# Performance work log

Measured on AMD Instinct MI355X. Metric: run time of the kernel, lower is better.

## Reference

```python
import jax, jax.numpy as jnp
import numpy as np
from jax import lax

KS = 11          # kernel_size
SIGMA = 1.5
MAX_VAL = 1.0
K1, K2 = 0.01, 0.03


def _gauss2d(ks=KS, sigma=SIGMA):
    x = np.arange(ks, dtype=np.float64) - ks // 2
    g = np.exp(-(x ** 2) / (2.0 * sigma ** 2))
    g = g / g.sum()
    return np.outer(g, g).astype(np.float32)  # [ks, ks]


def _bilinear_matrix(n_in, n_out):
    # align_corners=True bilinear resize as a linear map [n_out, n_in]
    pos = np.arange(n_out, dtype=np.float64) * (n_in - 1) / (n_out - 1)
    i0 = np.floor(pos).astype(np.int64)
    i1 = np.minimum(i0 + 1, n_in - 1)
    w = (pos - i0).astype(np.float32)
    M = np.zeros((n_out, n_in), dtype=np.float32)
    M[np.arange(n_out), i0] += 1.0 - w
    M[np.arange(n_out), i1] += w
    return jnp.asarray(M)


def setup_inputs() -> dict:
    key = jax.random.key(0)
    k1, k2 = jax.random.split(key)
    inp = jax.random.uniform(k1, (32, 3, 384, 384), dtype=jnp.float32)
    tgt = jax.random.uniform(k2, (32, 3, 512, 512), dtype=jnp.float32)
    return {"input": inp, "target": tgt}


def _ssim_loss(input, target):
    B, C, Hi, Wi = input.shape
    Ho, Wo = target.shape[-2], target.shape[-1]
    # bilinear align_corners interpolation of input to target spatial size
    A = _bilinear_matrix(Hi, Ho)  # [Ho, Hi]
    Bm = _bilinear_matrix(Wi, Wo)  # [Wo, Wi]
    img1 = jnp.einsum('oh,bchw,pw->bcop', A, input, Bm)
    img2 = target

    w2d = jnp.asarray(_gauss2d())
    window = jnp.broadcast_to(w2d, (C, 1, KS, KS))  # depthwise kernel [C,1,k,k]

    def dwconv(x):
        return lax.conv_general_dilated(
            x, window, window_strides=(1, 1), padding='VALID',
            feature_group_count=C,
            dimension_numbers=('NCHW', 'OIHW', 'NCHW'))

    mu1 = dwconv(img1)
    mu2 = dwconv(img2)
    mu1_sq = mu1 * mu1
    mu2_sq = mu2 * mu2
    mu1_mu2 = mu1 * mu2
    sigma1_sq = dwconv(img1 * img1) - mu1_sq
    sigma2_sq = dwconv(img2 * img2) - mu2_sq
    sigma12 = dwconv(img1 * img2) - mu1_mu2

    C1 = (K1 * MAX_VAL) ** 2
    C2 = (K2 * MAX_VAL) ** 2
    v1 = 2.0 * sigma12 + C2
    v2 = sigma1_sq + sigma2_sq + C2
    ssim_map = (2.0 * mu1_mu2 + C1) * v1 / ((mu1_sq + mu2_sq + C1) * v2)
    ret = jnp.mean(ssim_map)
    return jnp.clip(1.0 - ret, 0.0, 1.0)


def reference(input, target):
    return _ssim_loss(input, target)
```

## Files before the change

### kernel.cpp

```cpp
#include <hip/hip_runtime.h>


constexpr int KS = 11;
constexpr int HI = 384, WI = 384, HO = 512, WO = 512;
constexpr int OUTD = 502;
constexpr int NPLANE = 96;
constexpr int CH_OUT = 32;
constexpr int NCHUNK = 16;
constexpr float C1 = 1.0e-4f;
constexpr float C2 = 9.0e-4f;

__device__ __constant__ float GW[KS] = {
    0.00102838f, 0.00759876f, 0.03600076f, 0.10936070f, 0.21300554f,
    0.26601172f, 0.21300554f, 0.10936070f, 0.03600076f, 0.00759876f, 0.00102838f};

__device__ __forceinline__ float4 f4fma(float w, float4 x, float4 a)
{
    a.x = fmaf(w, x.x, a.x); a.y = fmaf(w, x.y, a.y);
    a.z = fmaf(w, x.z, a.z); a.w = fmaf(w, x.w, a.w);
    return a;
}

__device__ __forceinline__ float ssim_term(float4 f)
{
    float S = f.x, D = f.y, P = f.z, M = f.w;
    float SS = S * S, DD = D * D;
    float mu12 = 0.25f * (SS - DD);
    float musq = 0.5f  * (SS + DD);
    float s12  = 0.25f * (P - M) - mu12;
    float ssum = 0.5f  * (P + M) - musq;
    float num = fmaf(2.f, mu12, C1) * fmaf(2.f, s12, C2);
    float den = (musq + C1) * (ssum + C2);
    return __fdividef(num, den);
}

__global__ __launch_bounds__(256, 2)
void ssim_stream(const float* __restrict__ input, const float* __restrict__ target,
                 double* __restrict__ accum)
{
    __shared__ __align__(16) float4 chE[2][262];
    __shared__ __align__(16) float4 chO[2][262];
    __shared__ float wave_sums[4];

    const int tid   = threadIdx.x;
    const int chunk = blockIdx.x;
    const int plane = blockIdx.y;
    const int oyb   = chunk * CH_OUT;
    const int nout  = min(CH_OUT, OUTD - oyb);
    const int rows  = nout + KS - 1;

    const int c0 = 2 * tid;

    float pA = (float)(c0 * (WI - 1)) / (float)(WO - 1);
    int   xA0 = (int)pA; float wxA = pA - (float)xA0;
    float pB = (float)((c0 + 1) * (WI - 1)) / (float)(WO - 1);
    int   xB0 = (int)pB; float wxB = pB - (float)xB0;
    const bool shift = (xB0 != xA0);
    const int xs0 = xA0, xs1 = xA0 + 1, xs2 = min(xA0 + 2, WI - 1);

    const float* __restrict__ ip = input  + (size_t)plane * HI * WI;
    const float* __restrict__ tp = target + (size_t)plane * HO * WO;

    float4 rA[11], rB[11];
    #pragma unroll
    for (int s = 0; s < 11; ++s) {
        rA[s] = make_float4(0.f, 0.f, 0.f, 0.f);
        rB[s] = make_float4(0.f, 0.f, 0.f, 0.f);
    }

    float u0[2], u1[2], u2[2], v0[2], v1[2], v2[2], wyp[2];
    float2 tg[2];
    auto PRELOAD = [&](int r, int sl) {
        int y = oyb + r;
        float py = (float)(y * (HI - 1)) / (float)(HO - 1);
        int y0 = (int)py; wyp[sl] = py - (float)y0;
        int y1 = min(y0 + 1, HI - 1);
        const float* r0 = ip + y0 * WI;
        const float* r1 = ip + y1 * WI;
        u0[sl] = r0[xs0]; u1[sl] = r0[xs1]; u2[sl] = r0[xs2];
        v0[sl] = r1[xs0]; v1[sl] = r1[xs1]; v2[sl] = r1[xs2];
        tg[sl] = *(const float2*)&tp[y * WO + c0];
    };

    float lsum = 0.f;
    PRELOAD(0, 0);
    PRELOAD(1, 1);

    for (int t = 0; t < 2; ++t) {
        #pragma unroll
        for (int i = 0; i < 22; ++i) {
            const int r = t * 22 + i;
            if (r < rows) {
                const int p = i & 1;
                float wy = wyp[p];
                float V0 = fmaf(wy, v0[p] - u0[p], u0[p]);
                float V1 = fmaf(wy, v1[p] - u1[p], u1[p]);
                float V2 = fmaf(wy, v2[p] - u2[p], u2[p]);
                float a0 = fmaf(wxA, V1 - V0, V0);
                float bL = shift ? V1 : V0;
                float bR = shift ? V2 : V1;
                float a1 = fmaf(wxB, bR - bL, bL);
                float2 tv = tg[p];
                float s0 = a0 + tv.x, d0 = a0 - tv.x;
                float s1 = a1 + tv.y, d1 = a1 - tv.y;
                chE[p][tid] = make_float4(s0, d0, s0 * s0, d0 * d0);
                chO[p][tid] = make_float4(s1, d1, s1 * s1, d1 * d1);
                if (r + 2 < rows) PRELOAD(r + 2, p);
                __syncthreads();
                float4 acc0 = make_float4(0.f, 0.f, 0.f, 0.f);
                float4 acc1 = make_float4(0.f, 0.f, 0.f, 0.f);
                #pragma unroll
                for (int m = 0; m < 6; ++m) {
                    float4 E = chE[p][tid + m];
                    float4 O = chO[p][tid + m];
                    float we = GW[2 * m];
                    acc0 = f4fma(we, E, acc0);
                    acc1 = f4fma(we, O, acc1);
                    if (m < 5) acc0 = f4fma(GW[2 * m + 1], O, acc0);
                    if (m >= 1) acc1 = f4fma(GW[2 * m - 1], E, acc1);
                }
                const int im = i % 11;
                #pragma unroll
                for (int j = 0; j < 11; ++j) {
                    const int sl = (im - j + 11) % 11;
                    rA[sl] = f4fma(GW[j], acc0, rA[sl]);
                    rB[sl] = f4fma(GW[j], acc1, rB[sl]);
                }
                const int sf = (im + 1) % 11;
                if (r >= 10) {
                    if (c0 < OUTD) {
                        lsum += ssim_term(rA[sf]);
                        if (c0 + 1 < OUTD) lsum += ssim_term(rB[sf]);
                    }
                }
                rA[sf] = make_float4(0.f, 0.f, 0.f, 0.f);
                rB[sf] = make_float4(0.f, 0.f, 0.f, 0.f);
            }
        }
    }

    #pragma unroll
    for (int off = 32; off > 0; off >>= 1) lsum += __shfl_down(lsum, off);
    int wave = tid >> 6, lane = tid & 63;
    if (lane == 0) wave_sums[wave] = lsum;
    __syncthreads();
    if (tid == 0) {
        float s = wave_sums[0] + wave_sums[1] + wave_sums[2] + wave_sums[3];
        atomicAdd(accum, (double)s);
    }
}

__global__ void ssim_finalize(const double* __restrict__ accum, float* __restrict__ out)
{
    if (threadIdx.x == 0 && blockIdx.x == 0) {
        double mean = accum[0] / ((double)NPLANE * OUTD * OUTD);
        double l = 1.0 - mean;
        if (l < 0.0) l = 0.0;
        if (l > 1.0) l = 1.0;
        out[0] = (float)l;
    }
}

extern "C" void kernel_launch(void* const* d_in, const int* in_sizes, int n_in,
                              void* d_out, int out_size, void* d_ws, size_t ws_size,
                              hipStream_t stream)
{
    const float* input  = (const float*)d_in[0];
    const float* target = (const float*)d_in[1];
    float* out = (float*)d_out;
    double* accum = (double*)d_ws;

    hipMemsetAsync(accum, 0, sizeof(double), stream);

    dim3 grid(NCHUNK, NPLANE);
    ssim_stream<<<grid, dim3(256), 0, stream>>>(input, target, accum);
    ssim_finalize<<<1, 64, 0, stream>>>(accum, out);
}
```

Before: 309.1 us.

## Do vertical blur first from a register ring, horizontal via LDS

Reorders the separable Gaussian so each thread keeps a ring of 11 raw sum/difference rows in registers and applies the vertical filter first. Only the resulting vertical sums are exchanged through LDS for the horizontal pass. This replaces the 11-slot sliding accumulator arrays (two float4 arrays) with a single float4 ring, cutting register pressure so the launch bound can ask for 4 blocks per SM instead of 2. The trade-off is that each output row now recomputes an 11-tap vertical sum including squares, and the first 10 rows skip the barrier and LDS work.

```diff
diff --git a/kernel.cpp b/kernel.cpp
--- a/kernel.cpp
+++ b/kernel.cpp
@@ -34,12 +34,12 @@
     return __fdividef(num, den);
 }
 
-__global__ __launch_bounds__(256, 2)
+__global__ __launch_bounds__(256, 4)
 void ssim_stream(const float* __restrict__ input, const float* __restrict__ target,
                  double* __restrict__ accum)
 {
-    __shared__ __align__(16) float4 chE[2][262];
-    __shared__ __align__(16) float4 chO[2][262];
+    __shared__ __align__(16) float4 hE[2][262];
+    __shared__ __align__(16) float4 hO[2][262];
     __shared__ float wave_sums[4];
 
     const int tid   = threadIdx.x;
@@ -56,17 +56,12 @@
     float pB = (float)((c0 + 1) * (WI - 1)) / (float)(WO - 1);
     int   xB0 = (int)pB; float wxB = pB - (float)xB0;
     const bool shift = (xB0 != xA0);
-    const int xs0 = xA0, xs1 = xA0 + 1, xs2 = min(xA0 + 2, WI - 1);
+    const int xs0 = xA0, xs1 = min(xA0 + 1, WI - 1), xs2 = min(xA0 + 2, WI - 1);
 
     const float* __restrict__ ip = input  + (size_t)plane * HI * WI;
     const float* __restrict__ tp = target + (size_t)plane * HO * WO;
 
-    float4 rA[11], rB[11];
-    #pragma unroll
-    for (int s = 0; s < 11; ++s) {
-        rA[s] = make_float4(0.f, 0.f, 0.f, 0.f);
-        rB[s] = make_float4(0.f, 0.f, 0.f, 0.f);
-    }
+    float4 q[11];
 
     float u0[2], u1[2], u2[2], v0[2], v1[2], v2[2], wyp[2];
     float2 tg[2];
@@ -91,7 +86,8 @@
         for (int i = 0; i < 22; ++i) {
             const int r = t * 22 + i;
             if (r < rows) {
-                const int p = i & 1;
+                const int p  = i & 1;
+                const int im = i % 11;
                 float wy = wyp[p];
                 float V0 = fmaf(wy, v0[p] - u0[p], u0[p]);
                 float V1 = fmaf(wy, v1[p] - u1[p], u1[p]);
@@ -101,40 +97,41 @@
                 float bR = shift ? V2 : V1;
                 float a1 = fmaf(wxB, bR - bL, bL);
                 float2 tv = tg[p];
-                float s0 = a0 + tv.x, d0 = a0 - tv.x;
-                float s1 = a1 + tv.y, d1 = a1 - tv.y;
-                chE[p][tid] = make_float4(s0, d0, s0 * s0, d0 * d0);
-                chO[p][tid] = make_float4(s1, d1, s1 * s1, d1 * d1);
+                q[im] = make_float4(a0 + tv.x, a0 - tv.x, a1 + tv.y, a1 - tv.y);
                 if (r + 2 < rows) PRELOAD(r + 2, p);
-                __syncthreads();
-                float4 acc0 = make_float4(0.f, 0.f, 0.f, 0.f);
-                float4 acc1 = make_float4(0.f, 0.f, 0.f, 0.f);
-                #pragma unroll
-                for (int m = 0; m < 6; ++m) {
-                    float4 E = chE[p][tid + m];
-                    float4 O = chO[p][tid + m];
-                    float we = GW[2 * m];
-                    acc0 = f4fma(we, E, acc0);
-                    acc1 = f4fma(we, O, acc1);
-                    if (m < 5) acc0 = f4fma(GW[2 * m + 1], O, acc0);
-                    if (m >= 1) acc1 = f4fma(GW[2 * m - 1], E, acc1);
-                }
-                const int im = i % 11;
-                #pragma unroll
-                for (int j = 0; j < 11; ++j) {
-                    const int sl = (im - j + 11) % 11;
-                    rA[sl] = f4fma(GW[j], acc0, rA[sl]);
-                    rB[sl] = f4fma(GW[j], acc1, rB[sl]);
-                }
-                const int sf = (im + 1) % 11;
-                if (r >= 10) {
+                if (r >= KS - 1) {
+                    float4 accA = make_float4(0.f, 0.f, 0.f, 0.f);
+                    float4 accB = make_float4(0.f, 0.f, 0.f, 0.f);
+                    #pragma unroll
+                    for (int j = 0; j < KS; ++j) {
+                        const int sl = (im + 1 + j) % 11;
+                        float4 x = q[sl];
+                        float4 x2 = make_float4(x.x * x.x, x.y * x.y,
+                                                x.z * x.z, x.w * x.w);
+                        float w = GW[j];
+                        accA = f4fma(w, x,  accA);
+                        accB = f4fma(w, x2, accB);
+                    }
+                    hE[p][tid] = make_float4(accA.x, accA.y, accB.x, accB.y);
+                    hO[p][tid] = make_float4(accA.z, accA.w, accB.z, accB.w);
+                    __syncthreads();
+                    float4 o0 = make_float4(0.f, 0.f, 0.f, 0.f);
+                    float4 o1 = make_float4(0.f, 0.f, 0.f, 0.f);
+                    #pragma unroll
+                    for (int m = 0; m < 6; ++m) {
+                        float4 E = hE[p][tid + m];
+                        float4 O = hO[p][tid + m];
+                        float we = GW[2 * m];
+                        o0 = f4fma(we, E, o0);
+                        o1 = f4fma(we, O, o1);
+                        if (m < 5)  o0 = f4fma(GW[2 * m + 1], O, o0);
+                        if (m >= 1) o1 = f4fma(GW[2 * m - 1], E, o1);
+                    }
                     if (c0 < OUTD) {
-                        lsum += ssim_term(rA[sf]);
-                        if (c0 + 1 < OUTD) lsum += ssim_term(rB[sf]);
+                        lsum += ssim_term(o0);
+                        if (c0 + 1 < OUTD) lsum += ssim_term(o1);
                     }
                 }
-                rA[sf] = make_float4(0.f, 0.f, 0.f, 0.f);
-                rB[sf] = make_float4(0.f, 0.f, 0.f, 0.f);
             }
         }
     }
```

Result: faster. 301.2 us (-2.6%).
